# Optimization experiments

Measured on AMD Instinct MI355X. Metric: run time of the kernel, lower is better.

## Reference

```python
import jax, jax.numpy as jnp
import numpy as np

N_NODES = 10000
N_EDGES = 320000
F_IN = 256
F_OUT = 256


def setup_inputs() -> dict:
    key = jax.random.key(0)
    k1, k2, k3 = jax.random.split(key, 3)
    X = jax.random.normal(k1, (N_NODES, F_IN), dtype=jnp.float32)
    # kaiming-normal init: std = sqrt(2 / fan_in)
    W = jax.random.normal(k2, (F_IN, F_OUT), dtype=jnp.float32) * np.float32(np.sqrt(2.0 / F_IN))
    edge_list = jax.random.randint(k3, (2, N_EDGES), 0, N_NODES, dtype=jnp.int64 if jax.config.jax_enable_x64 else jnp.int32)
    return {"X": X, "W": W, "edge_list": edge_list}


def reference(X, W, edge_list):
    # Faithful to the original: build dense adjacency from edge list
    # (duplicate edges collapse to 1 via set-semantics), add self-loops,
    # symmetric degree normalization D^{-1/2} A_hat D^{-1/2}, then X @ W, ReLU.
    n = X.shape[0]
    src, tgt = edge_list[0], edge_list[1]
    A = jnp.zeros((n, n), dtype=X.dtype).at[src, tgt].set(1.0)  # [N, N]
    A_hat = A + jnp.eye(n, dtype=X.dtype)
    deg = jnp.sum(A_hat, axis=0)                # column sums (in-degree + 1)
    d_inv_sqrt = 1.0 / jnp.sqrt(deg)            # diag(D)^-1 then sqrt == 1/sqrt(deg)
    # D_normed @ A_hat @ D_normed == d[:,None] * A_hat * d[None,:]
    norm_adj = A_hat * d_inv_sqrt[:, None] * d_inv_sqrt[None, :]
    z = norm_adj @ (X @ W)                      # [N, N] @ [N, F_out]
    return jax.nn.relu(z)
```

## Files before the change

kernel.cpp:

```cpp
#include <hip/hip_runtime.h>
#include <hip/hip_bf16.h>


constexpr int N = 10000;
constexpr int E = 320000;
constexpr int F = 256;
constexpr int DEGCAP = 96;
constexpr int GROWS = 25;
constexpr int NG = N / GROWS;
constexpr int EPB = 2048;
constexpr int BCAP = 28;
constexpr int REG_PB = NG * BCAP;

constexpr int BKT_BLKS  = (E + EPB - 1) / EPB;
constexpr int GEMM_BLKS = (N + 31) / 32;

constexpr size_t OFF_DEG  = 0;
constexpr size_t OFF_CNT  = 40960;
constexpr size_t OFF_ADJ  = 81920;
constexpr size_t OFF_WT   = OFF_ADJ + 4ull * N * DEGCAP;
constexpr size_t OFF_H    = OFF_WT + 2ull * F * F;
constexpr size_t OFF_REG  = OFF_H + 2ull * N * F;
constexpr size_t OFF_PART = OFF_REG + 4ull * BKT_BLKS * REG_PB;

typedef short s8v __attribute__((ext_vector_type(8)));
typedef float f4v __attribute__((ext_vector_type(4)));
typedef unsigned u4v __attribute__((ext_vector_type(4)));

__device__ __forceinline__ float bf2f(unsigned short u) {
    union { unsigned u; float f; } c; c.u = (unsigned)u << 16; return c.f;
}
__device__ __forceinline__ unsigned short f2bf(float f) {
    union { __hip_bfloat16 b; unsigned short s; } c; c.b = __float2bfloat16(f); return c.s;
}

__global__ void k_pre(const float* __restrict__ W, unsigned short* __restrict__ Wt) {
    __shared__ unsigned short ls[4][F];
    int n0 = blockIdx.x * 4;
    int k = threadIdx.x;
    float4 v = *(const float4*)&W[k * F + n0];
    ls[0][k] = f2bf(v.x); ls[1][k] = f2bf(v.y);
    ls[2][k] = f2bf(v.z); ls[3][k] = f2bf(v.w);
    __syncthreads();
    int nn = threadIdx.x >> 6;
    int kk = (threadIdx.x & 63) * 4;
    uint2 o;
    o.x = (unsigned)ls[nn][kk]     | ((unsigned)ls[nn][kk + 1] << 16);
    o.y = (unsigned)ls[nn][kk + 2] | ((unsigned)ls[nn][kk + 3] << 16);
    *(uint2*)&Wt[(n0 + nn) * F + kk] = o;
}

__global__ void __launch_bounds__(512) k_bucket_gemm(
    const int* __restrict__ edges, int* __restrict__ region,
    const float* __restrict__ X, const unsigned short* __restrict__ Wt,
    unsigned short* __restrict__ H) {
    __shared__ union U {
        struct { int bkt[NG][BCAP]; int bcnt[NG]; } b;
        unsigned short lsA[32][264];
    } sh;
    int tid = threadIdx.x;

    if (blockIdx.x < BKT_BLKS) {
        int probe = edges[2 * (tid & 63) + 1];
        bool is32 = __ballot(probe != 0) != 0ull;
        for (int i = tid; i < NG; i += 512) sh.b.bcnt[i] = 0;
        int4 mone; mone.x = -1; mone.y = -1; mone.z = -1; mone.w = -1;
        int4* b4 = (int4*)&sh.b.bkt[0][0];
        for (int i = tid; i < REG_PB / 4; i += 512) b4[i] = mone;
        __syncthreads();
#pragma unroll
        for (int k = 0; k < EPB / 512; ++k) {
            int e = blockIdx.x * EPB + k * 512 + tid;
            if (e >= E) break;
            int s, t;
            if (is32) { s = edges[e];     t = edges[E + e]; }
            else      { s = edges[2 * e]; t = edges[2 * E + 2 * e]; }
            if ((unsigned)s < (unsigned)N && (unsigned)t < (unsigned)N) {
                int g = s / GROWS;
                int v = ((s - g * GROWS) << 14) | t;
                int pos = atomicAdd(&sh.b.bcnt[g], 1);
                if (pos < BCAP) sh.b.bkt[g][pos] = v;
            }
        }
        __syncthreads();
        int4* dst = (int4*)(region + (size_t)blockIdx.x * REG_PB);
        for (int i = tid; i < REG_PB / 4; i += 512) dst[i] = b4[i];
        return;
    }
    int r0 = (blockIdx.x - BKT_BLKS) * 32;
    {
        int row = tid >> 4, seg = tid & 15;
        if (r0 + row < N) {
            const float4* src = (const float4*)(X + (r0 + row) * F + seg * 16);
#pragma unroll
            for (int j = 0; j < 4; ++j) {
                float4 v = src[j];
                uint2 o;
                o.x = (unsigned)f2bf(v.x) | ((unsigned)f2bf(v.y) << 16);
                o.y = (unsigned)f2bf(v.z) | ((unsigned)f2bf(v.w) << 16);
                *(uint2*)&sh.lsA[row][seg * 16 + j * 4] = o;
            }
        }
    }
    __syncthreads();
    int lane = tid & 63, wv = tid >> 6;
    int sl = wv >> 2;
    int cg = wv & 3;
    if (r0 + sl * 16 >= N) return;
    int m = lane & 15, q = lane >> 4;
    const s8v* B = (const s8v*)(Wt + m * F + q * 8);
    f4v acc[4] = {};
#pragma unroll
    for (int kk = 0; kk < 8; ++kk) {
        s8v af = *(const s8v*)&sh.lsA[sl * 16 + m][kk * 32 + q * 8];
#pragma unroll
        for (int tt = 0; tt < 4; ++tt) {
            int t = cg * 4 + tt;
            s8v bf = B[t * 512 + kk * 4];
            acc[tt] = __builtin_amdgcn_mfma_f32_16x16x32_bf16(af, bf, acc[tt], 0, 0, 0);
        }
    }
#pragma unroll
    for (int tt = 0; tt < 4; ++tt) {
        int col = (cg * 4 + tt) * 16 + m;
#pragma unroll
        for (int i = 0; i < 4; ++i)
            H[(r0 + sl * 16 + q * 4 + i) * F + col] = f2bf(acc[tt][i]);
    }
}

__global__ void __launch_bounds__(512) k_fillscan(
    const int* __restrict__ region,
    int* __restrict__ adj, int* __restrict__ cnt, unsigned* __restrict__ part32) {
    __shared__ unsigned bmp[GROWS][320];
    __shared__ unsigned hist32[N / 4];
    int tid = threadIdx.x;
    {
        u4v z = {0u, 0u, 0u, 0u};
        u4v* z4 = (u4v*)&bmp[0][0];
        for (int i = tid; i < GROWS * 320 / 4; i += 512) z4[i] = z;
        u4v* h4 = (u4v*)hist32;
        for (int i = tid; i < N / 16; i += 512) h4[i] = z;
    }
    __syncthreads();

    int g = blockIdx.x;
    const u4v* reg4 = (const u4v*)region;
    for (int idx = tid; idx < BKT_BLKS * (BCAP / 4); idx += 512) {
        int j = idx / (BCAP / 4), q = idx - (BCAP / 4) * j;
        u4v v4 = reg4[(size_t)j * (REG_PB / 4) + g * (BCAP / 4) + q];
#pragma unroll
        for (int jj = 0; jj < 4; ++jj) {
            int v = (int)v4[jj];
            if (v >= 0) {
                int r = v >> 14;
                unsigned t = (unsigned)(v & 16383);
                atomicOr(&bmp[r][t >> 5], 1u << (t & 31));
            }
        }
    }
    __syncthreads();

    int wave = tid >> 6, lane = tid & 63;
    for (int r = wave; r < GROWS; r += 8) {
        int s = g * GROWS + r;
        const unsigned* row = bmp[r];
        unsigned w0 = row[lane];
        unsigned w1 = row[lane + 64];
        unsigned w2 = row[lane + 128];
        unsigned w3 = row[lane + 192];
        unsigned w4 = row[lane + 256];
        int pc = __popc(w0) + __popc(w1) + __popc(w2) + __popc(w3) + __popc(w4);
        int sc = pc;
#pragma unroll
        for (int d = 1; d < 64; d <<= 1) {
            int v = __shfl_up(sc, d);
            if (lane >= d) sc += v;
        }
        int o = sc - pc;
        if (lane == 63) cnt[s] = sc < DEGCAP ? sc : DEGCAP;
        int* arow = adj + s * DEGCAP;
        unsigned wvs[5] = {w0, w1, w2, w3, w4};
#pragma unroll
        for (int j = 0; j < 5; ++j) {
            unsigned w = wvs[j];
            int base = (j * 64 + lane) * 32;
            while (w) {
                int b = __ffs(w) - 1;
                w &= w - 1;
                int t = base + b;
                if (o < DEGCAP) arow[o] = t;
                ++o;
                atomicAdd(&hist32[t >> 2], 1u << ((t & 3) * 8));
            }
        }
    }
    __syncthreads();
    {
        u4v* src = (u4v*)hist32;
        u4v* dst = (u4v*)(part32 + (size_t)g * (N / 4));
        for (int i = tid; i < N / 16; i += 512) dst[i] = src[i];
    }
}

__global__ void k_deg(const unsigned* __restrict__ part32, int* __restrict__ deg) {
    int j2 = blockIdx.x * blockDim.x + threadIdx.x;
    if (j2 >= N / 4) return;
    int s0 = 1, s1 = 1, s2 = 1, s3 = 1;
#pragma unroll 8
    for (int b = 0; b < NG; ++b) {
        unsigned w = part32[(size_t)b * (N / 4) + j2];
        s0 += w & 255; s1 += (w >> 8) & 255; s2 += (w >> 16) & 255; s3 += w >> 24;
    }
    int4 o; o.x = s0; o.y = s1; o.z = s2; o.w = s3;
    *(int4*)&deg[j2 * 4] = o;
}

#define ACC8(hv, dv)                                          \
    p0 += dv * bf2f((unsigned short)(hv.x & 0xFFFF));         \
    p1 += dv * bf2f((unsigned short)(hv.x >> 16));            \
    p2 += dv * bf2f((unsigned short)(hv.y & 0xFFFF));         \
    p3 += dv * bf2f((unsigned short)(hv.y >> 16));            \
    p4 += dv * bf2f((unsigned short)(hv.z & 0xFFFF));         \
    p5 += dv * bf2f((unsigned short)(hv.z >> 16));            \
    p6 += dv * bf2f((unsigned short)(hv.w & 0xFFFF));         \
    p7 += dv * bf2f((unsigned short)(hv.w >> 16));

__global__ void k_gather(const int* __restrict__ adj, const int* __restrict__ cnt,
                         const int* __restrict__ deg,
                         const unsigned short* __restrict__ H,
                         float* __restrict__ out) {
    int wave = threadIdx.x >> 6;
    int lane = threadIdx.x & 63;
    int s = blockIdx.x * 4 + wave;
    int half = lane >> 5, hl = lane & 31;
    const uint4* H16 = (const uint4*)H;
    float ds = rsqrtf((float)deg[s]);
    int c = cnt[s]; if (c > DEGCAP) c = DEGCAP;
    const int* a = adj + s * DEGCAP;
    int tl = 0; float dl = 0.0f;
    if (lane < c) { tl = a[lane]; dl = rsqrtf((float)deg[tl]); }

    uint4 hs = H16[s * 32 + hl];
    float p0, p1, p2, p3, p4, p5, p6, p7;
    {
        float w = half ? 0.0f : ds;
        p0 = w * bf2f((unsigned short)(hs.x & 0xFFFF));
        p1 = w * bf2f((unsigned short)(hs.x >> 16));
        p2 = w * bf2f((unsigned short)(hs.y & 0xFFFF));
        p3 = w * bf2f((unsigned short)(hs.y >> 16));
        p4 = w * bf2f((unsigned short)(hs.z & 0xFFFF));
        p5 = w * bf2f((unsigned short)(hs.z >> 16));
        p6 = w * bf2f((unsigned short)(hs.w & 0xFFFF));
        p7 = w * bf2f((unsigned short)(hs.w >> 16));
    }
    int cc = c < 64 ? c : 64;
    for (int i = 0; i < cc; i += 8) {
        int i0 = i + half, i1 = i + 2 + half, i2 = i + 4 + half, i3 = i + 6 + half;
        int t0 = __shfl(tl, i0), t1 = __shfl(tl, i1);
        int t2 = __shfl(tl, i2), t3 = __shfl(tl, i3);
        float d0 = __shfl(dl, i0), d1 = __shfl(dl, i1);
        float d2 = __shfl(dl, i2), d3 = __shfl(dl, i3);
        uint4 h0 = H16[t0 * 32 + hl];
        uint4 h1 = H16[t1 * 32 + hl];
        uint4 h2 = H16[t2 * 32 + hl];
        uint4 h3 = H16[t3 * 32 + hl];
        ACC8(h0, d0) ACC8(h1, d1) ACC8(h2, d2) ACC8(h3, d3)
    }
    for (int i = 64; i < c; ++i) {
        int t = a[i];
        float d = half ? 0.0f : rsqrtf((float)deg[t]);
        uint4 h = H16[t * 32 + hl];
        ACC8(h, d)
    }
    p0 += __shfl(p0, lane ^ 32); p1 += __shfl(p1, lane ^ 32);
    p2 += __shfl(p2, lane ^ 32); p3 += __shfl(p3, lane ^ 32);
    p4 += __shfl(p4, lane ^ 32); p5 += __shfl(p5, lane ^ 32);
    p6 += __shfl(p6, lane ^ 32); p7 += __shfl(p7, lane ^ 32);
    p0 = fmaxf(p0 * ds, 0.0f); p1 = fmaxf(p1 * ds, 0.0f);
    p2 = fmaxf(p2 * ds, 0.0f); p3 = fmaxf(p3 * ds, 0.0f);
    p4 = fmaxf(p4 * ds, 0.0f); p5 = fmaxf(p5 * ds, 0.0f);
    p6 = fmaxf(p6 * ds, 0.0f); p7 = fmaxf(p7 * ds, 0.0f);
    float4 o;
    if (half) { o.x = p4; o.y = p5; o.z = p6; o.w = p7; }
    else      { o.x = p0; o.y = p1; o.z = p2; o.w = p3; }
    ((float4*)out)[s * 64 + hl * 2 + half] = o;
}

extern "C" void kernel_launch(void* const* d_in, const int* in_sizes, int n_in,
                              void* d_out, int out_size, void* d_ws, size_t ws_size,
                              hipStream_t stream) {
    const float* X = (const float*)d_in[0];
    const float* W = (const float*)d_in[1];
    const int* edges = (const int*)d_in[2];

    char* ws = (char*)d_ws;
    int* deg           = (int*)(ws + OFF_DEG);
    int* cnt           = (int*)(ws + OFF_CNT);
    int* adj           = (int*)(ws + OFF_ADJ);
    unsigned short* Wt = (unsigned short*)(ws + OFF_WT);
    unsigned short* H  = (unsigned short*)(ws + OFF_H);
    int* region        = (int*)(ws + OFF_REG);
    unsigned* part32   = (unsigned*)(ws + OFF_PART);

    k_pre<<<64, 256, 0, stream>>>(W, Wt);
    k_bucket_gemm<<<BKT_BLKS + GEMM_BLKS, 512, 0, stream>>>(edges, region, X, Wt, H);
    k_fillscan<<<NG, 512, 0, stream>>>(region, adj, cnt, part32);
    k_deg<<<(N / 4 + 255) / 256, 256, 0, stream>>>(part32, deg);
    k_gather<<<N / 4, 256, 0, stream>>>(adj, cnt, deg, H, (float*)d_out);
}
```

Measured before the change: 127.0 us.

## Split H into two 128-column planes and gather per plane

```diff
diff --git a/kernel.cpp b/kernel.cpp
--- a/kernel.cpp
+++ b/kernel.cpp
@@ -123,9 +123,11 @@
 #pragma unroll
     for (int tt = 0; tt < 4; ++tt) {
         int col = (cg * 4 + tt) * 16 + m;
+        int plane = col >> 7, c128 = col & 127;
 #pragma unroll
         for (int i = 0; i < 4; ++i)
-            H[(r0 + sl * 16 + q * 4 + i) * F + col] = f2bf(acc[tt][i]);
+            H[((size_t)plane * N + (r0 + sl * 16 + q * 4 + i)) * 128 + c128] =
+                f2bf(acc[tt][i]);
     }
 }
 
@@ -232,19 +234,18 @@
                          float* __restrict__ out) {
     int wave = threadIdx.x >> 6;
     int lane = threadIdx.x & 63;
-    int s = blockIdx.x * 4 + wave;
-    int half = lane >> 5, hl = lane & 31;
-    const uint4* H16 = (const uint4*)H;
+    int plane = blockIdx.x / 2500;
+    int s = (blockIdx.x % 2500) * 4 + wave;
+    int gq = lane >> 4, hl = lane & 15;
+    const uint4* Hp = (const uint4*)(H + (size_t)plane * N * 128);
     float ds = rsqrtf((float)deg[s]);
     int c = cnt[s]; if (c > DEGCAP) c = DEGCAP;
     const int* a = adj + s * DEGCAP;
-    int tl = 0; float dl = 0.0f;
-    if (lane < c) { tl = a[lane]; dl = rsqrtf((float)deg[tl]); }
-
-    uint4 hs = H16[s * 32 + hl];
+
+    uint4 hs = Hp[s * 16 + hl];
     float p0, p1, p2, p3, p4, p5, p6, p7;
     {
-        float w = half ? 0.0f : ds;
+        float w = (gq == 0) ? ds : 0.0f;
         p0 = w * bf2f((unsigned short)(hs.x & 0xFFFF));
         p1 = w * bf2f((unsigned short)(hs.x >> 16));
         p2 = w * bf2f((unsigned short)(hs.y & 0xFFFF));
@@ -254,25 +255,17 @@
         p6 = w * bf2f((unsigned short)(hs.w & 0xFFFF));
         p7 = w * bf2f((unsigned short)(hs.w >> 16));
     }
-    int cc = c < 64 ? c : 64;
-    for (int i = 0; i < cc; i += 8) {
-        int i0 = i + half, i1 = i + 2 + half, i2 = i + 4 + half, i3 = i + 6 + half;
-        int t0 = __shfl(tl, i0), t1 = __shfl(tl, i1);
-        int t2 = __shfl(tl, i2), t3 = __shfl(tl, i3);
-        float d0 = __shfl(dl, i0), d1 = __shfl(dl, i1);
-        float d2 = __shfl(dl, i2), d3 = __shfl(dl, i3);
-        uint4 h0 = H16[t0 * 32 + hl];
-        uint4 h1 = H16[t1 * 32 + hl];
-        uint4 h2 = H16[t2 * 32 + hl];
-        uint4 h3 = H16[t3 * 32 + hl];
-        ACC8(h0, d0) ACC8(h1, d1) ACC8(h2, d2) ACC8(h3, d3)
-    }
-    for (int i = 64; i < c; ++i) {
-        int t = a[i];
-        float d = half ? 0.0f : rsqrtf((float)deg[t]);
-        uint4 h = H16[t * 32 + hl];
+    for (int i = 0; i < c; i += 4) {
+        int idx = i + gq;
+        int t = s; float d = 0.0f;
+        if (idx < c) { t = a[idx]; d = rsqrtf((float)deg[t]); }
+        uint4 h = Hp[t * 16 + hl];
         ACC8(h, d)
     }
+    p0 += __shfl(p0, lane ^ 16); p1 += __shfl(p1, lane ^ 16);
+    p2 += __shfl(p2, lane ^ 16); p3 += __shfl(p3, lane ^ 16);
+    p4 += __shfl(p4, lane ^ 16); p5 += __shfl(p5, lane ^ 16);
+    p6 += __shfl(p6, lane ^ 16); p7 += __shfl(p7, lane ^ 16);
     p0 += __shfl(p0, lane ^ 32); p1 += __shfl(p1, lane ^ 32);
     p2 += __shfl(p2, lane ^ 32); p3 += __shfl(p3, lane ^ 32);
     p4 += __shfl(p4, lane ^ 32); p5 += __shfl(p5, lane ^ 32);
@@ -281,10 +274,14 @@
     p2 = fmaxf(p2 * ds, 0.0f); p3 = fmaxf(p3 * ds, 0.0f);
     p4 = fmaxf(p4 * ds, 0.0f); p5 = fmaxf(p5 * ds, 0.0f);
     p6 = fmaxf(p6 * ds, 0.0f); p7 = fmaxf(p7 * ds, 0.0f);
-    float4 o;
-    if (half) { o.x = p4; o.y = p5; o.z = p6; o.w = p7; }
-    else      { o.x = p0; o.y = p1; o.z = p2; o.w = p3; }
-    ((float4*)out)[s * 64 + hl * 2 + half] = o;
+    float* orow = out + (size_t)s * F + plane * 128;
+    if (gq == 0) {
+        float4 o; o.x = p0; o.y = p1; o.z = p2; o.w = p3;
+        *(float4*)&orow[hl * 8] = o;
+    } else if (gq == 1) {
+        float4 o; o.x = p4; o.y = p5; o.z = p6; o.w = p7;
+        *(float4*)&orow[hl * 8 + 4] = o;
+    }
 }
 
 extern "C" void kernel_launch(void* const* d_in, const int* in_sizes, int n_in,
@@ -307,5 +304,5 @@
     k_bucket_gemm<<<BKT_BLKS + GEMM_BLKS, 512, 0, stream>>>(edges, region, X, Wt, H);
     k_fillscan<<<NG, 512, 0, stream>>>(region, adj, cnt, part32);
     k_deg<<<(N / 4 + 255) / 256, 256, 0, stream>>>(part32, deg);
-    k_gather<<<N / 4, 256, 0, stream>>>(adj, cnt, deg, H, (float*)d_out);
-}
+    k_gather<<<5000, 256, 0, stream>>>(adj, cnt, deg, H, (float*)d_out);
+}
```

Result: slower. 137.6 us (+8.4%).
